# Performance work log

Hardware: AMD Instinct MI355X
Metric: run time of the kernel (lower is better)

## Reference

```python
import jax, jax.numpy as jnp
import numpy as np

LOG1000 = 6.9077542789816375  # ln(1000)


def setup_inputs() -> dict:
    key = jax.random.key(0)
    kx, kp = jax.random.split(key)
    x = jax.random.normal(kx, (65536, 128), dtype=jnp.float32)
    points = jax.random.normal(kp, (2048, 128), dtype=jnp.float32)
    beta_raw = jnp.array([-3.5], dtype=jnp.float32)
    return {"x": x, "points": points, "beta_raw": beta_raw}


def reference(x, points, beta_raw):
    t1 = jnp.sum(x * x, axis=-1, keepdims=True)            # [N, 1]
    t2 = jnp.sum(points * points, axis=-1)[None, :]        # [1, P]
    t3 = 2.0 * jnp.einsum('nd,pd->np', x, points)          # [N, P]
    d2 = jnp.clip(t1 + t2 - t3, 0.0)
    min_d = jnp.min(d2, axis=-1)                           # [N]
    # translated sigmoid
    beta = jax.nn.softplus(beta_raw)                       # [1]
    alpha = -beta * LOG1000
    return jax.nn.sigmoid((min_d + alpha) / beta)
```

## Files before the change

### kernel.cpp

```cpp
#include <hip/hip_runtime.h>


#define NROWS 65536
#define NPTS  2048
#define DIMS  128
#define LOG1000F 6.9077542789816375f

typedef __attribute__((ext_vector_type(8))) int i32x8;
typedef __attribute__((ext_vector_type(4))) float f32x4;

union AFrag { int d[8]; i32x8 v; };
union BFrag { uint4 u4[2]; i32x8 v; };

__global__ __launch_bounds__(256) void prep_points_kernel(
    const float* __restrict__ pts, unsigned char* __restrict__ ptsf8,
    float* __restrict__ pnorm)
{
    int tid  = threadIdx.x;
    int lane = tid & 63;
    int w    = tid >> 6;
    int pt   = blockIdx.x * 4 + w;
    const float2 v = *reinterpret_cast<const float2*>(
        pts + (size_t)pt * DIMS + lane * 2);
    int pk = __builtin_amdgcn_cvt_pk_fp8_f32(v.x, v.y, 0, false);
    int T  = pt >> 4, pm = pt & 15;
    int q  = lane >> 4;
    int c  = (lane >> 3) & 1;
    int j  = (lane & 7) * 2;
    size_t dst = (size_t)((T * 2 + c) * 64 + q * 16 + pm) * 16 + j;
    *reinterpret_cast<unsigned short*>(ptsf8 + dst) =
        (unsigned short)(pk & 0xFFFF);
    float ss = v.x * v.x + v.y * v.y;
    ss += __shfl_xor(ss, 1, 64);
    ss += __shfl_xor(ss, 2, 64);
    ss += __shfl_xor(ss, 4, 64);
    ss += __shfl_xor(ss, 8, 64);
    ss += __shfl_xor(ss, 16, 64);
    ss += __shfl_xor(ss, 32, 64);
    if (lane == 0) pnorm[pt] = ss;
}

__global__ __launch_bounds__(256, 2) void distnet_main_kernel(
    const float* __restrict__ x, const unsigned char* __restrict__ ptsf8,
    const float* __restrict__ pnorm, const float* __restrict__ beta_raw,
    float* __restrict__ out)
{
    __shared__ __align__(16) float s_pn[NPTS];
    __shared__ float s_red[4][64];
    __shared__ float s_xn[64];

    int tid = threadIdx.x;
    {
        const float4* p4 = reinterpret_cast<const float4*>(pnorm);
        float4* d4 = reinterpret_cast<float4*>(s_pn);
        float4 a = p4[tid], b = p4[tid + 256];
        d4[tid]       = make_float4(-.5f*a.x, -.5f*a.y, -.5f*a.z, -.5f*a.w);
        d4[tid + 256] = make_float4(-.5f*b.x, -.5f*b.y, -.5f*b.z, -.5f*b.w);
    }

    int wid   = tid >> 6, lane = tid & 63;
    int m     = lane & 15, q = lane >> 4;
    int rbase = blockIdx.x * 64;

    AFrag afrag[4];
#pragma unroll
    for (int t = 0; t < 4; ++t) {
        const float* xp = x + (size_t)(rbase + t * 16 + m) * DIMS + q * 32;
        float s = 0.f;
#pragma unroll
        for (int d = 0; d < 8; ++d) {
            float4 v = *reinterpret_cast<const float4*>(xp + d * 4);
            int w0 = __builtin_amdgcn_cvt_pk_fp8_f32(v.x, v.y, 0, false);
            w0 = __builtin_amdgcn_cvt_pk_fp8_f32(v.z, v.w, w0, true);
            afrag[t].d[d] = w0;
            s += v.x * v.x + v.y * v.y + v.z * v.z + v.w * v.w;
        }
        s += __shfl_xor(s, 16, 64);
        s += __shfl_xor(s, 32, 64);
        if (wid == 0 && q == 0) s_xn[t * 16 + m] = s;
    }
    __syncthreads();

    float runmax[4][4];
#pragma unroll
    for (int t = 0; t < 4; ++t)
#pragma unroll
        for (int r = 0; r < 4; ++r) runmax[t][r] = -1e30f;

    const uint4* bsw = reinterpret_cast<const uint4*>(ptsf8);
    const int T0 = wid * 32;

    BFrag bA, bB, bC, bD;
    float pnA, pnB, pnC, pnD;

#define LOADT(gT, buf, pnh) do {                       \
        buf.u4[0] = bsw[(gT) * 128 + lane];            \
        buf.u4[1] = bsw[(gT) * 128 + 64 + lane];       \
        pnh = s_pn[(gT) * 16 + m];                     \
    } while (0)

    auto compute = [&](const BFrag& buf, float pnh) {
#pragma unroll
        for (int t = 0; t < 4; ++t) {
            f32x4 acc = {pnh, pnh, pnh, pnh};
            acc = __builtin_amdgcn_mfma_scale_f32_16x16x128_f8f6f4(
                afrag[t].v, buf.v, acc, 0, 0, 0, 0x7F7F7F7F, 0, 0x7F7F7F7F);
#pragma unroll
            for (int r = 0; r < 4; ++r)
                runmax[t][r] = fmaxf(runmax[t][r], acc[r]);
        }
    };

    LOADT(T0 + 0, bA, pnA);
    LOADT(T0 + 1, bB, pnB);
    LOADT(T0 + 2, bC, pnC);
    LOADT(T0 + 3, bD, pnD);
#pragma unroll 1
    for (int T = 0; T < 28; T += 4) {
        compute(bA, pnA);
        LOADT(T0 + T + 4, bA, pnA);
        compute(bB, pnB);
        LOADT(T0 + T + 5, bB, pnB);
        compute(bC, pnC);
        LOADT(T0 + T + 6, bC, pnC);
        compute(bD, pnD);
        LOADT(T0 + T + 7, bD, pnD);
    }
    compute(bA, pnA);
    compute(bB, pnB);
    compute(bC, pnC);
    compute(bD, pnD);
#undef LOADT

#pragma unroll
    for (int t = 0; t < 4; ++t) {
#pragma unroll
        for (int r = 0; r < 4; ++r) {
            float v = runmax[t][r];
            v = fminf(v, v);
            v = fmaxf(v, __shfl_xor(v, 1, 64));
            v = fmaxf(v, __shfl_xor(v, 2, 64));
            v = fmaxf(v, __shfl_xor(v, 4, 64));
            v = fmaxf(v, __shfl_xor(v, 8, 64));
            if (m == 0)
                s_red[wid][t * 16 + q * 4 + r] = v;
        }
    }
    __syncthreads();

    if (tid < 64) {
        float vmax  = fmaxf(fmaxf(s_red[0][tid], s_red[1][tid]),
                            fmaxf(s_red[2][tid], s_red[3][tid]));
        float d2    = fmaxf(fmaf(-2.f, vmax, s_xn[tid]), 0.f);
        float br    = beta_raw[0];
        float beta  = log1pf(expf(br));
        float alpha = -beta * LOG1000F;
        float z     = (d2 + alpha) / beta;
        out[(size_t)rbase + tid] = 1.f / (1.f + expf(-z));
    }
}

extern "C" void kernel_launch(void* const* d_in, const int* in_sizes, int n_in,
                              void* d_out, int out_size, void* d_ws, size_t ws_size,
                              hipStream_t stream) {
    const float* x        = (const float*)d_in[0];
    const float* pts      = (const float*)d_in[1];
    const float* beta_raw = (const float*)d_in[2];
    float* out            = (float*)d_out;

    unsigned char* ptsf8 = (unsigned char*)d_ws;
    float* pnorm = (float*)((char*)d_ws + (size_t)NPTS * DIMS);

    prep_points_kernel<<<NPTS / 4, 256, 0, stream>>>(pts, ptsf8, pnorm);
    distnet_main_kernel<<<NROWS / 64, 256, 0, stream>>>(x, ptsf8, pnorm,
                                                        beta_raw, out);
}
```

Measured before the change: 103.2 us.

## Widen main kernel to 512 threads covering two row groups per block

Each block now processes 128 rows with 8 waves, two row groups sharing the same point-norm LDS table, and the grid is halved. This amortizes the per-block point-norm load and scaling over twice as many rows. Point-fragment addressing is rewritten as a pointer advanced each iteration instead of recomputing indices, and a redundant fminf in the reduction is dropped. Occupancy changes because launch bounds now request 512 threads with 2 blocks per CU, which limits the registers available to each thread.

```diff
diff --git a/kernel.cpp b/kernel.cpp
--- a/kernel.cpp
+++ b/kernel.cpp
@@ -40,27 +40,27 @@
     if (lane == 0) pnorm[pt] = ss;
 }
 
-__global__ __launch_bounds__(256, 2) void distnet_main_kernel(
+__global__ __launch_bounds__(512, 2) void distnet_main_kernel(
     const float* __restrict__ x, const unsigned char* __restrict__ ptsf8,
     const float* __restrict__ pnorm, const float* __restrict__ beta_raw,
     float* __restrict__ out)
 {
     __shared__ __align__(16) float s_pn[NPTS];
-    __shared__ float s_red[4][64];
-    __shared__ float s_xn[64];
+    __shared__ float s_red[4][128];
+    __shared__ float s_xn[128];
 
     int tid = threadIdx.x;
     {
         const float4* p4 = reinterpret_cast<const float4*>(pnorm);
-        float4* d4 = reinterpret_cast<float4*>(s_pn);
-        float4 a = p4[tid], b = p4[tid + 256];
-        d4[tid]       = make_float4(-.5f*a.x, -.5f*a.y, -.5f*a.z, -.5f*a.w);
-        d4[tid + 256] = make_float4(-.5f*b.x, -.5f*b.y, -.5f*b.z, -.5f*b.w);
+        float4 a = p4[tid];
+        reinterpret_cast<float4*>(s_pn)[tid] =
+            make_float4(-.5f*a.x, -.5f*a.y, -.5f*a.z, -.5f*a.w);
     }
 
-    int wid   = tid >> 6, lane = tid & 63;
-    int m     = lane & 15, q = lane >> 4;
-    int rbase = blockIdx.x * 64;
+    int wid  = tid >> 6, lane = tid & 63;
+    int m    = lane & 15, q = lane >> 4;
+    int rg   = wid >> 2, pg = wid & 3;
+    int rbase = blockIdx.x * 128 + rg * 64;
 
     AFrag afrag[4];
 #pragma unroll
@@ -77,7 +77,7 @@
         }
         s += __shfl_xor(s, 16, 64);
         s += __shfl_xor(s, 32, 64);
-        if (wid == 0 && q == 0) s_xn[t * 16 + m] = s;
+        if (pg == 0 && q == 0) s_xn[rg * 64 + t * 16 + m] = s;
     }
     __syncthreads();
 
@@ -87,16 +87,17 @@
 #pragma unroll
         for (int r = 0; r < 4; ++r) runmax[t][r] = -1e30f;
 
-    const uint4* bsw = reinterpret_cast<const uint4*>(ptsf8);
-    const int T0 = wid * 32;
+    const char*  bp  = (const char*)ptsf8 + (size_t)(pg * 32) * 2048
+                       + (size_t)lane * 16;
+    const float* pnp = s_pn + pg * 32 * 16 + m;
 
     BFrag bA, bB, bC, bD;
     float pnA, pnB, pnC, pnD;
 
-#define LOADT(gT, buf, pnh) do {                       \
-        buf.u4[0] = bsw[(gT) * 128 + lane];            \
-        buf.u4[1] = bsw[(gT) * 128 + 64 + lane];       \
-        pnh = s_pn[(gT) * 16 + m];                     \
+#define LOADT(rel, buf, pnh) do {                                          \
+        buf.u4[0] = *reinterpret_cast<const uint4*>(bp + (rel) * 2048);    \
+        buf.u4[1] = *reinterpret_cast<const uint4*>(bp + (rel) * 2048 + 1024);\
+        pnh = pnp[(rel) * 16];                                             \
     } while (0)
 
     auto compute = [&](const BFrag& buf, float pnh) {
@@ -111,20 +112,22 @@
         }
     };
 
-    LOADT(T0 + 0, bA, pnA);
-    LOADT(T0 + 1, bB, pnB);
-    LOADT(T0 + 2, bC, pnC);
-    LOADT(T0 + 3, bD, pnD);
+    LOADT(0, bA, pnA);
+    LOADT(1, bB, pnB);
+    LOADT(2, bC, pnC);
+    LOADT(3, bD, pnD);
 #pragma unroll 1
-    for (int T = 0; T < 28; T += 4) {
+    for (int it = 0; it < 7; ++it) {
         compute(bA, pnA);
-        LOADT(T0 + T + 4, bA, pnA);
+        LOADT(4, bA, pnA);
         compute(bB, pnB);
-        LOADT(T0 + T + 5, bB, pnB);
+        LOADT(5, bB, pnB);
         compute(bC, pnC);
-        LOADT(T0 + T + 6, bC, pnC);
+        LOADT(6, bC, pnC);
         compute(bD, pnD);
-        LOADT(T0 + T + 7, bD, pnD);
+        LOADT(7, bD, pnD);
+        bp  += 4 * 2048;
+        pnp += 4 * 16;
     }
     compute(bA, pnA);
     compute(bB, pnB);
@@ -137,18 +140,17 @@
 #pragma unroll
         for (int r = 0; r < 4; ++r) {
             float v = runmax[t][r];
-            v = fminf(v, v);
             v = fmaxf(v, __shfl_xor(v, 1, 64));
             v = fmaxf(v, __shfl_xor(v, 2, 64));
             v = fmaxf(v, __shfl_xor(v, 4, 64));
             v = fmaxf(v, __shfl_xor(v, 8, 64));
             if (m == 0)
-                s_red[wid][t * 16 + q * 4 + r] = v;
+                s_red[pg][rg * 64 + t * 16 + q * 4 + r] = v;
         }
     }
     __syncthreads();
 
-    if (tid < 64) {
+    if (tid < 128) {
         float vmax  = fmaxf(fmaxf(s_red[0][tid], s_red[1][tid]),
                             fmaxf(s_red[2][tid], s_red[3][tid]));
         float d2    = fmaxf(fmaf(-2.f, vmax, s_xn[tid]), 0.f);
@@ -156,7 +158,7 @@
         float beta  = log1pf(expf(br));
         float alpha = -beta * LOG1000F;
         float z     = (d2 + alpha) / beta;
-        out[(size_t)rbase + tid] = 1.f / (1.f + expf(-z));
+        out[(size_t)blockIdx.x * 128 + tid] = 1.f / (1.f + expf(-z));
     }
 }
 
@@ -172,6 +174,6 @@
     float* pnorm = (float*)((char*)d_ws + (size_t)NPTS * DIMS);
 
     prep_points_kernel<<<NPTS / 4, 256, 0, stream>>>(pts, ptsf8, pnorm);
-    distnet_main_kernel<<<NROWS / 64, 256, 0, stream>>>(x, ptsf8, pnorm,
-                                                        beta_raw, out);
+    distnet_main_kernel<<<NROWS / 128, 512, 0, stream>>>(x, ptsf8, pnorm,
+                                                         beta_raw, out);
 }
```

Result: no change. 103.9 us (+0.7%).
